# Kernel tuning notes

Hardware: AMD Instinct MI355X
Metric: run time of the kernel (lower is better)

Reference implementation:

```python
import jax, jax.numpy as jnp
import numpy as np

POOL_K = 8        # predictor_kernel_size
THRESH = 0.05     # predictor_threshold
EPS = 1e-5        # masked_fill value


def _round_ste(x):
    # straight-through round (forward: round)
    return x + jax.lax.stop_gradient(jnp.round(x) - x)


def _quant_act_uint(x, scale, bits):
    # Brevitas Uint8ActPerTensorFloat-style fake quant: unsigned, per-tensor scale
    n = 2.0 ** bits - 1.0
    return jnp.clip(_round_ste(x / scale), 0.0, n) * scale


def _quant_weight_per_oc(w, bits):
    # signed, narrow-range, per-output-channel scaling: s = max|w| / (2^(b-1)-1)
    n = 2.0 ** (bits - 1) - 1.0
    s = jnp.max(jnp.abs(w), axis=(1, 2, 3), keepdims=True) / n
    return jnp.clip(_round_ste(w / s), -n, n) * s


def _conv(x, w):
    return jax.lax.conv_general_dilated(
        x, w, window_strides=(1, 1), padding=((1, 1), (1, 1)),
        dimension_numbers=('NCHW', 'OIHW', 'NCHW'))


def _predictor_mask(x):
    # AvgPool2d(8) (stride=kernel) -> threshold -> nearest upsample back to HxW
    B, C, H, W = x.shape
    pooled = x.reshape(B, C, H // POOL_K, POOL_K, W // POOL_K, POOL_K).mean(axis=(3, 5))
    m = pooled >= THRESH
    m = jnp.repeat(jnp.repeat(m, POOL_K, axis=2), POOL_K, axis=3)  # nearest interp
    return jax.lax.stop_gradient(m)  # mask.detach()


def setup_inputs() -> dict:
    key = jax.random.key(0)
    k1, k2, k3 = jax.random.split(key, 3)
    x = jax.random.normal(k1, (32, 128, 56, 56), jnp.float32)
    w_high = jax.random.normal(k2, (128, 128, 3, 3), jnp.float32) * 0.05
    w_low = jax.random.normal(k3, (128, 128, 3, 3), jnp.float32) * 0.05
    return {
        'x': x,
        'w_high': w_high,
        'w_low': w_low,
        'act_scale_high': jnp.float32(0.02),
        'act_scale_low': jnp.float32(0.04),
    }


def reference(x, w_high, w_low, act_scale_high, act_scale_low):
    mask = _predictor_mask(x)                 # [B,C,H,W] bool
    x_high = jnp.where(mask, x, EPS)          # masked_fill(~mask, 1e-5)
    x_low = jnp.where(mask, EPS, x)           # masked_fill(mask, 1e-5)
    y_high = _conv(_quant_act_uint(x_high, act_scale_high, 8),
                   _quant_weight_per_oc(w_high, 8))
    y_low = _conv(_quant_act_uint(x_low, act_scale_low, 4),
                  _quant_weight_per_oc(w_low, 4))
    return y_high + y_low
```

## Files before the change

### kernel.cpp

```cpp
#include <hip/hip_runtime.h>
#include <hip/hip_bf16.h>
#include <stdint.h>

#define BATCH 32
#define CH 128
#define HH 56
#define WW 56
#define HW 3136
#define M_TOTAL (BATCH*HW)
#define PLANE ((size_t)M_TOTAL * 16)

using int4v   = __attribute__((ext_vector_type(4))) int;
using float4v = __attribute__((ext_vector_type(4))) float;

#define WQB_OFF 0
#define SCB_OFF 294912
#define ZP_OFF  296448
#define AQN_OFF 296704

#define GLD_LDS16(g, l)                                                        \
  __builtin_amdgcn_global_load_lds(                                            \
      (const __attribute__((address_space(1))) void*)(g),                      \
      (__attribute__((address_space(3))) void*)(l), 16, 0, 0)

#define KSTR 484

__global__ __launch_bounds__(256) void prep_kernel(
    const float* __restrict__ x,
    const float* __restrict__ wh, const float* __restrict__ wl,
    const float* __restrict__ p_sh, const float* __restrict__ p_sl,
    char* __restrict__ wqb, float* __restrict__ scb, int* __restrict__ zp,
    char* __restrict__ aqn) {
  __shared__ __align__(16) float smem[16 * KSTR + 128];
  int t = threadIdx.x;

  if (blockIdx.x >= BATCH * 7 * 8) {
    int blk = blockIdx.x - BATCH * 7 * 8;
    int which = blk >> 7, oc = blk & 127;
    if (blk == 0 && t < 64)
      zp[t] = (t < 32) ? 0x80808080 : 0;
    const float* src = (which ? wl : wh) + (size_t)oc * 1152;
    float n = which ? 7.0f : 127.0f;
    float* red = smem;
    int* ired = (int*)(smem + 256);

    float m = 0.0f;
    for (int e = t; e < 1152; e += 256) m = fmaxf(m, fabsf(src[e]));
    red[t] = m;
    __syncthreads();
    for (int s = 128; s > 0; s >>= 1) {
      if (t < s) red[t] = fmaxf(red[t], red[t + s]);
      __syncthreads();
    }
    float scale = red[0] / n;

    int partial = 0;
    for (int e = t; e < 1152; e += 256) {
      int tt = e >> 7, ic = e & 127;
      float q = rintf(src[ic * 9 + tt] / scale);
      q = fminf(fmaxf(q, -n), n);
      int k = (int)q;
      partial += k;
      wqb[((size_t)tt * 128 + oc) * 256 + which * 128 + ic] = (char)k;
    }
    ired[t] = partial;
    __syncthreads();
    for (int s = 128; s > 0; s >>= 1) {
      if (t < s) ired[t] += ired[t + s];
      __syncthreads();
    }
    if (t == 0) {
      float s_act = which ? p_sl[0] : p_sh[0];
      float sc = s_act * scale;
      if (which == 0) {
        scb[oc] = sc;
        scb[256 + oc] = sc * 128.0f * (float)ired[0];
      } else {
        scb[128 + oc] = sc;
      }
    }
    return;
  }

  int bi = blockIdx.x;
  int cg = bi & 7;
  int bb = bi >> 3;
  int b = bb / 7, band = bb - b * 7;
  float* sx = smem;
  float* smk = smem + 16 * KSTR;
  #pragma unroll
  for (int i = 0; i < 7; ++i) {
    int idx = i * 256 + t;
    int k = idx / 112, rem = idx - k * 112;
    int r = rem / 14, w4 = rem - r * 14;
    *(float4v*)(sx + k * KSTR + r * 60 + w4 * 4) =
        *(const float4v*)(x + ((size_t)(b * 128 + cg * 16 + k)) * HW
                            + (band * 8 + r) * 56 + w4 * 4);
  }
  __syncthreads();
  if (t < 112) {
    int k = t / 7, bw = t - (t / 7) * 7;
    float s = 0.0f;
    #pragma unroll
    for (int r = 0; r < 8; ++r)
      #pragma unroll
      for (int j = 0; j < 8; ++j)
        s += sx[k * KSTR + r * 60 + bw * 8 + j];
    smk[t] = (s * (1.0f / 64.0f) >= 0.05f) ? 1.0f : 0.0f;
  }
  __syncthreads();
  float shs = p_sh[0], sls = p_sl[0];
  #pragma unroll
  for (int it = 0; it < 2; ++it) {
    int pos = it * 256 + t;
    if (pos < 448) {
      int r = pos / 56, w = pos - r * 56;
      int h = band * 8 + r;
      size_t gp = (size_t)b * HW + (size_t)h * 56 + w;
      int hw_[4] = {0, 0, 0, 0}, lw_[4] = {0, 0, 0, 0};
      int mcell = w >> 3;
      #pragma unroll
      for (int k = 0; k < 16; ++k) {
        float xv = sx[k * KSTR + r * 60 + w];
        bool mk = smk[k * 7 + mcell] != 0.0f;
        float xh = mk ? xv : 1e-5f;
        int kh = (int)fminf(fmaxf(rintf(xh / shs), 0.0f), 255.0f) - 128;
        float xl = mk ? 1e-5f : xv;
        int kl = (int)fminf(fmaxf(rintf(xl / sls), 0.0f), 15.0f);
        hw_[k >> 2] |= (kh & 0xff) << ((k & 3) * 8);
        lw_[k >> 2] |= (kl & 0xff) << ((k & 3) * 8);
      }
      *(int4v*)(aqn + ((size_t)cg * M_TOTAL + gp) * 16) =
          (int4v){hw_[0], hw_[1], hw_[2], hw_[3]};
      *(int4v*)(aqn + ((size_t)(8 + cg) * M_TOTAL + gp) * 16) =
          (int4v){lw_[0], lw_[1], lw_[2], lw_[3]};
    }
  }
}

__global__ __launch_bounds__(256, 2) void conv_mfma_kernel(
    const char* __restrict__ wqb,
    const char* __restrict__ aqn,
    const char* __restrict__ zp,
    const float* __restrict__ scb,
    float* __restrict__ out) {
  __shared__ __align__(16) char As[3][144 * 64];
  __shared__ __align__(16) char Bs[3][192 * 64];

  int tid = threadIdx.x;
  int lane = tid & 63, wv = tid >> 6;
  int wm = wv >> 1, wn = wv & 1;
  int lr = lane & 15, quad = lane >> 4;
  int bx = blockIdx.x;
  int m0 = (((bx & 7) * 98) + (bx >> 3)) * 128;
  int oc0 = blockIdx.y * 64;

  int ng = (wv == 0) ? 3 : 2;
  int sgrp[3] = {wv, wv + 4, wv + 8};
  const char* abase[3];
  const char* zbase[3];
  int avalid[3], ah[3];
  #pragma unroll
  for (int j = 0; j < 3; ++j) {
    int slot = sgrp[j] * 16 + (lane >> 2);
    int q = ((lane & 3) ^ (slot >> 1)) & 3;
    int p = m0 + slot - 8;
    int pv = (p >= 0) && (p < M_TOTAL);
    int pc = pv ? p : 0;
    int bb = pc / HW, rem = pc - bb * HW;
    int hh = rem / 56;
    abase[j] = aqn + (size_t)q * PLANE + (size_t)pc * 16;
    zbase[j] = zp + q * 16;
    avalid[j] = pv;
    ah[j] = hh;
  }
  const char* bbase[3];
  #pragma unroll
  for (int i = 0; i < 3; ++i) {
    int slot = wv * 48 + i * 16 + (lane >> 2);
    int qp = (((lane & 3) ^ (slot >> 1)) & 3) * 16;
    int dwi_s = slot >> 6, ocr = slot & 63;
    bbase[i] = wqb + ((size_t)(dwi_s * 128 + oc0 + ocr)) * 256 + qp;
  }
  int lo_ok[4], hi_ok[4];
  #pragma unroll
  for (int mi = 0; mi < 4; ++mi) {
    int m = m0 + wm * 64 + mi * 16 + lr;
    int w = (m % HW) % 56;
    lo_ok[mi] = (w > 0);
    hi_ok[mi] = (w < 55);
  }

  int4v acch[4][2], accl[4][2];
  #pragma unroll
  for (int mi = 0; mi < 4; ++mi)
    #pragma unroll
    for (int ni = 0; ni < 2; ++ni) {
      acch[mi][ni] = (int4v){0, 0, 0, 0};
      accl[mi][ni] = (int4v){0, 0, 0, 0};
    }

  auto stage = [&](int s, char* A, char* B) {
    int dh3 = s >> 2, icc = s & 3;
    int dh = dh3 - 1;
    #pragma unroll
    for (int j = 0; j < 3; ++j) {
      if (j < ng) {
        int h2 = ah[j] + dh;
        bool ok = avalid[j] && ((unsigned)h2 < (unsigned)HH);
        const char* p = ok ? (abase[j] + dh * (56 * 16) + (size_t)icc * (4 * PLANE))
                           : (zbase[j] + icc * 64);
        GLD_LDS16(p, A + sgrp[j] * 1024);
      }
    }
    #pragma unroll
    for (int i = 0; i < 3; ++i)
      GLD_LDS16(bbase[i] + (size_t)dh3 * 98304 + icc * 64,
                B + (wv * 48 + i * 16) * 64);
  };

  auto compute = [&](int s, const char* A, const char* B) {
    int icc = s & 3;
    const bool high = (icc < 2);
    const int patv = high ? (int)0x80808080 : 0;
    const int4v pat = (int4v){patv, patv, patv, patv};
    #pragma unroll
    for (int dwi = 0; dwi < 3; ++dwi) {
      int4v af[4], bf[2];
      #pragma unroll
      for (int mi = 0; mi < 4; ++mi) {
        int sA = wm * 64 + mi * 16 + lr + 7 + dwi;
        af[mi] = *(const int4v*)(A + sA * 64 + (((quad ^ (sA >> 1)) & 3) * 16));
        bool ok = (dwi == 1) | (dwi == 0 ? lo_ok[mi] : hi_ok[mi]);
        af[mi] = ok ? af[mi] : pat;
      }
      #pragma unroll
      for (int ni = 0; ni < 2; ++ni) {
        int sB = dwi * 64 + wn * 32 + ni * 16 + lr;
        bf[ni] = *(const int4v*)(B + sB * 64 + (((quad ^ (sB >> 1)) & 3) * 16));
      }
      __builtin_amdgcn_s_setprio(1);
      if (high) {
        #pragma unroll
        for (int mi = 0; mi < 4; ++mi)
          #pragma unroll
          for (int ni = 0; ni < 2; ++ni)
            acch[mi][ni] = __builtin_amdgcn_mfma_i32_16x16x64_i8(
                af[mi], bf[ni], acch[mi][ni], 0, 0, 0);
      } else {
        #pragma unroll
        for (int mi = 0; mi < 4; ++mi)
          #pragma unroll
          for (int ni = 0; ni < 2; ++ni)
            accl[mi][ni] = __builtin_amdgcn_mfma_i32_16x16x64_i8(
                af[mi], bf[ni], accl[mi][ni], 0, 0, 0);
      }
      __builtin_amdgcn_s_setprio(0);
    }
  };

  stage(0, As[0], Bs[0]);
  stage(1, As[1], Bs[1]);
  #pragma unroll
  for (int s = 0; s < 12; ++s) {
    if (s == 11) {
      asm volatile("s_waitcnt vmcnt(0)" ::: "memory");
    } else if (wv == 0) {
      asm volatile("s_waitcnt vmcnt(6)" ::: "memory");
    } else {
      asm volatile("s_waitcnt vmcnt(5)" ::: "memory");
    }
    __builtin_amdgcn_s_barrier();
    __builtin_amdgcn_sched_barrier(0);
    compute(s, As[s % 3], Bs[s % 3]);
    if (s < 10) stage(s + 2, As[(s + 2) % 3], Bs[(s + 2) % 3]);
  }

  #pragma unroll
  for (int mi = 0; mi < 4; ++mi) {
    int m = m0 + wm * 64 + mi * 16 + quad * 4;
    int b = m / HW, r = m - b * HW;
    float* obase = out + (size_t)b * (CH * HW) + r;
    #pragma unroll
    for (int ni = 0; ni < 2; ++ni) {
      int oc = oc0 + wn * 32 + ni * 16 + lr;
      float sch = scb[oc], scl = scb[128 + oc], bs = scb[256 + oc];
      float4v f;
      #pragma unroll
      for (int rg = 0; rg < 4; ++rg)
        f[rg] = sch * (float)acch[mi][ni][rg] + scl * (float)accl[mi][ni][rg] + bs;
      __builtin_nontemporal_store(f, (float4v*)(obase + (size_t)oc * HW));
    }
  }
}

extern "C" void kernel_launch(void* const* d_in, const int* in_sizes, int n_in,
                              void* d_out, int out_size, void* d_ws, size_t ws_size,
                              hipStream_t stream) {
  const float* x  = (const float*)d_in[0];
  const float* wh = (const float*)d_in[1];
  const float* wl = (const float*)d_in[2];
  const float* sh = (const float*)d_in[3];
  const float* sl = (const float*)d_in[4];
  float* out = (float*)d_out;

  char* ws = (char*)d_ws;
  char* wqb  = ws + WQB_OFF;
  float* scb = (float*)(ws + SCB_OFF);
  int* zp    = (int*)(ws + ZP_OFF);
  char* aqn  = ws + AQN_OFF;

  prep_kernel<<<dim3(BATCH * 7 * 8 + 256), dim3(256), 0, stream>>>(
      x, wh, wl, sh, sl, wqb, scb, zp, aqn);
  conv_mfma_kernel<<<dim3(M_TOTAL / 128, 2), dim3(256), 0, stream>>>(
      wqb, aqn, (const char*)zp, scb, out);
}
```

Baseline: 159.0 us.

## Use padded-width virtual rows to drop per-fragment boundary masking in conv

The GEMM M dimension now runs over a virtual layout where each row has one extra zero column (57 wide). Horizontal-neighbour taps past a row edge then land on a zero-point pad slot loaded at staging time, so the per-fragment lo/hi select in the MFMA inner loop goes away. Output stores become scalar, masked, non-vectorised writes that skip the pad column. The B buffer shrinks from triple to double buffering, with the wait counts adjusted, to allow 3 blocks per CU. This adds about 2% extra tiles of work and gives up the vectorised nontemporal stores.

```diff
diff --git a/kernel.cpp b/kernel.cpp
--- a/kernel.cpp
+++ b/kernel.cpp
@@ -8,6 +8,10 @@
 #define WW 56
 #define HW 3136
 #define M_TOTAL (BATCH*HW)
+#define WP 57
+#define HWP (HH*WP)
+#define MP_TOTAL (BATCH*HWP)
+#define NTILE (MP_TOTAL/128)
 #define PLANE ((size_t)M_TOTAL * 16)
 
 using int4v   = __attribute__((ext_vector_type(4))) int;
@@ -138,21 +142,23 @@
   }
 }
 
-__global__ __launch_bounds__(256, 2) void conv_mfma_kernel(
+__global__ __launch_bounds__(256, 3) void conv_mfma_kernel(
     const char* __restrict__ wqb,
     const char* __restrict__ aqn,
     const char* __restrict__ zp,
     const float* __restrict__ scb,
     float* __restrict__ out) {
   __shared__ __align__(16) char As[3][144 * 64];
-  __shared__ __align__(16) char Bs[3][192 * 64];
+  __shared__ __align__(16) char Bs[2][192 * 64];
 
   int tid = threadIdx.x;
   int lane = tid & 63, wv = tid >> 6;
   int wm = wv >> 1, wn = wv & 1;
   int lr = lane & 15, quad = lane >> 4;
   int bx = blockIdx.x;
-  int m0 = (((bx & 7) * 98) + (bx >> 3)) * 128;
+  int xcd = bx & 7, jj = bx >> 3;
+  int tile = (xcd < 6 ? xcd * 100 : 600 + (xcd - 6) * 99) + jj;
+  int m0 = tile * 128;
   int oc0 = blockIdx.y * 64;
 
   int ng = (wv == 0) ? 3 : 2;
@@ -165,13 +171,14 @@
     int slot = sgrp[j] * 16 + (lane >> 2);
     int q = ((lane & 3) ^ (slot >> 1)) & 3;
     int p = m0 + slot - 8;
-    int pv = (p >= 0) && (p < M_TOTAL);
+    int pv = (p >= 0) && (p < MP_TOTAL);
     int pc = pv ? p : 0;
-    int bb = pc / HW, rem = pc - bb * HW;
-    int hh = rem / 56;
-    abase[j] = aqn + (size_t)q * PLANE + (size_t)pc * 16;
+    int bb = pc / HWP, rem = pc - bb * HWP;
+    int hh = rem / WP, wp = rem - hh * WP;
+    int idx = (bb * HH + hh) * WW + wp;
+    abase[j] = aqn + (size_t)q * PLANE + (size_t)idx * 16;
     zbase[j] = zp + q * 16;
-    avalid[j] = pv;
+    avalid[j] = pv && (wp < WW);
     ah[j] = hh;
   }
   const char* bbase[3];
@@ -182,14 +189,6 @@
     int dwi_s = slot >> 6, ocr = slot & 63;
     bbase[i] = wqb + ((size_t)(dwi_s * 128 + oc0 + ocr)) * 256 + qp;
   }
-  int lo_ok[4], hi_ok[4];
-  #pragma unroll
-  for (int mi = 0; mi < 4; ++mi) {
-    int m = m0 + wm * 64 + mi * 16 + lr;
-    int w = (m % HW) % 56;
-    lo_ok[mi] = (w > 0);
-    hi_ok[mi] = (w < 55);
-  }
 
   int4v acch[4][2], accl[4][2];
   #pragma unroll
@@ -200,7 +199,7 @@
       accl[mi][ni] = (int4v){0, 0, 0, 0};
     }
 
-  auto stage = [&](int s, char* A, char* B) {
+  auto stageA = [&](int s, char* A) {
     int dh3 = s >> 2, icc = s & 3;
     int dh = dh3 - 1;
     #pragma unroll
@@ -213,6 +212,9 @@
         GLD_LDS16(p, A + sgrp[j] * 1024);
       }
     }
+  };
+  auto stageB = [&](int s, char* B) {
+    int dh3 = s >> 2, icc = s & 3;
     #pragma unroll
     for (int i = 0; i < 3; ++i)
       GLD_LDS16(bbase[i] + (size_t)dh3 * 98304 + icc * 64,
@@ -222,8 +224,6 @@
   auto compute = [&](int s, const char* A, const char* B) {
     int icc = s & 3;
     const bool high = (icc < 2);
-    const int patv = high ? (int)0x80808080 : 0;
-    const int4v pat = (int4v){patv, patv, patv, patv};
     #pragma unroll
     for (int dwi = 0; dwi < 3; ++dwi) {
       int4v af[4], bf[2];
@@ -231,8 +231,6 @@
       for (int mi = 0; mi < 4; ++mi) {
         int sA = wm * 64 + mi * 16 + lr + 7 + dwi;
         af[mi] = *(const int4v*)(A + sA * 64 + (((quad ^ (sA >> 1)) & 3) * 16));
-        bool ok = (dwi == 1) | (dwi == 0 ? lo_ok[mi] : hi_ok[mi]);
-        af[mi] = ok ? af[mi] : pat;
       }
       #pragma unroll
       for (int ni = 0; ni < 2; ++ni) {
@@ -259,37 +257,48 @@
     }
   };
 
-  stage(0, As[0], Bs[0]);
-  stage(1, As[1], Bs[1]);
+  stageA(0, As[0]);
+  stageB(0, Bs[0]);
+  stageA(1, As[1]);
   #pragma unroll
   for (int s = 0; s < 12; ++s) {
     if (s == 11) {
       asm volatile("s_waitcnt vmcnt(0)" ::: "memory");
     } else if (wv == 0) {
-      asm volatile("s_waitcnt vmcnt(6)" ::: "memory");
+      asm volatile("s_waitcnt vmcnt(3)" ::: "memory");
     } else {
-      asm volatile("s_waitcnt vmcnt(5)" ::: "memory");
+      asm volatile("s_waitcnt vmcnt(2)" ::: "memory");
     }
     __builtin_amdgcn_s_barrier();
     __builtin_amdgcn_sched_barrier(0);
-    compute(s, As[s % 3], Bs[s % 3]);
-    if (s < 10) stage(s + 2, As[(s + 2) % 3], Bs[(s + 2) % 3]);
+    if (s < 11) stageB(s + 1, Bs[(s + 1) & 1]);
+    compute(s, As[s % 3], Bs[s & 1]);
+    if (s < 10) stageA(s + 2, As[(s + 2) % 3]);
   }
 
   #pragma unroll
   for (int mi = 0; mi < 4; ++mi) {
-    int m = m0 + wm * 64 + mi * 16 + quad * 4;
-    int b = m / HW, r = m - b * HW;
-    float* obase = out + (size_t)b * (CH * HW) + r;
+    int p0 = m0 + wm * 64 + mi * 16 + quad * 4;
+    int valid[4];
+    size_t off[4];
+    #pragma unroll
+    for (int rg = 0; rg < 4; ++rg) {
+      int p = p0 + rg;
+      int b = p / HWP, rem = p - b * HWP;
+      int h = rem / WP, wp = rem - h * WP;
+      valid[rg] = (wp < WW);
+      off[rg] = (size_t)b * (CH * HW) + h * 56 + wp;
+    }
     #pragma unroll
     for (int ni = 0; ni < 2; ++ni) {
       int oc = oc0 + wn * 32 + ni * 16 + lr;
       float sch = scb[oc], scl = scb[128 + oc], bs = scb[256 + oc];
-      float4v f;
-      #pragma unroll
-      for (int rg = 0; rg < 4; ++rg)
-        f[rg] = sch * (float)acch[mi][ni][rg] + scl * (float)accl[mi][ni][rg] + bs;
-      __builtin_nontemporal_store(f, (float4v*)(obase + (size_t)oc * HW));
+      #pragma unroll
+      for (int rg = 0; rg < 4; ++rg) {
+        float f = sch * (float)acch[mi][ni][rg]
+                + scl * (float)accl[mi][ni][rg] + bs;
+        if (valid[rg]) out[off[rg] + (size_t)oc * HW] = f;
+      }
     }
   }
 }
@@ -312,6 +321,6 @@
 
   prep_kernel<<<dim3(BATCH * 7 * 8 + 256), dim3(256), 0, stream>>>(
       x, wh, wl, sh, sl, wqb, scb, zp, aqn);
-  conv_mfma_kernel<<<dim3(M_TOTAL / 128, 2), dim3(256), 0, stream>>>(
+  conv_mfma_kernel<<<dim3(NTILE, 2), dim3(256), 0, stream>>>(
       wqb, aqn, (const char*)zp, scb, out);
 }
```

Measured after the change: 177.2 us. 11.5% more time.
